# Kernel tuning notes

Hardware: AMD Instinct MI355X
Metric: run time of the kernel (lower is better)

The kernel has to match this reference:

```python
import jax, jax.numpy as jnp
import numpy as np

B, L, D, H = 2, 2048, 2048, 16
HD = D // H          # head_dim = 128
LD = HD // 4         # latent_dim = 32


def _linear_params(key, fan_in, fan_out):
    kw, kb = jax.random.split(key)
    bound = 1.0 / np.sqrt(fan_in)
    W = jax.random.uniform(kw, (fan_in, fan_out), jnp.float32, -bound, bound)
    b = jax.random.uniform(kb, (fan_out,), jnp.float32, -bound, bound)
    return W, b


def setup_inputs() -> dict:
    key = jax.random.key(0)
    ks = jax.random.split(key, 12)
    x = jax.random.normal(ks[0], (B, L, D), jnp.float32)
    cos = jax.random.uniform(ks[1], (L, HD // 2), jnp.float32)
    sin = jax.random.uniform(ks[2], (L, HD // 2), jnp.float32)
    Wq, bq = _linear_params(ks[3], D, D)
    Wk, bk = _linear_params(ks[4], D, D)
    Wv, bv = _linear_params(ks[5], D, D)
    Wqc, bqc = _linear_params(ks[6], HD, LD)
    Wkc, bkc = _linear_params(ks[7], HD, LD)
    Wvc, bvc = _linear_params(ks[8], HD, LD)
    Wd, bd = _linear_params(ks[9], LD, HD)
    Wo, bo = _linear_params(ks[10], D, D)
    return dict(x=x, cos=cos, sin=sin, Wq=Wq, bq=bq, Wk=Wk, bk=bk, Wv=Wv, bv=bv,
                Wqc=Wqc, bqc=bqc, Wkc=Wkc, bkc=bkc, Wvc=Wvc, bvc=bvc,
                Wd=Wd, bd=bd, Wo=Wo, bo=bo)


def _apply_rope(q, k, cos, sin):
    # q, k: (B, H, L, HD); cos, sin: (L, HD//2) -> broadcast over B, H
    c = cos[None, None, :, :]
    s = sin[None, None, :, :]
    qe, qo = q[..., ::2], q[..., 1::2]
    ke, ko = k[..., ::2], k[..., 1::2]
    q_rot = jnp.stack([qe * c - qo * s, qe * s + qo * c], axis=-1).reshape(q.shape)
    k_rot = jnp.stack([ke * c - ko * s, ke * s + ko * c], axis=-1).reshape(k.shape)
    return q_rot, k_rot


def reference(x, cos, sin, Wq, bq, Wk, bk, Wv, bv,
              Wqc, bqc, Wkc, bkc, Wvc, bvc, Wd, bd, Wo, bo):
    b, l, d = x.shape
    # projections -> (B, H, L, HD)
    q = (x @ Wq + bq).reshape(b, l, H, HD).transpose(0, 2, 1, 3)
    k = (x @ Wk + bk).reshape(b, l, H, HD).transpose(0, 2, 1, 3)
    v = (x @ Wv + bv).reshape(b, l, H, HD).transpose(0, 2, 1, 3)
    q, k = _apply_rope(q, k, cos, sin)
    # low-rank compression into latent_dim
    qc = jnp.einsum('bhld,de->bhle', q, Wqc) + bqc
    kc = jnp.einsum('bhld,de->bhle', k, Wkc) + bkc
    vc = jnp.einsum('bhld,de->bhle', v, Wvc) + bvc
    scores = jnp.einsum('bhqe,bhke->bhqk', qc, kc) / np.sqrt(LD).astype(np.float32)
    causal = jnp.tril(jnp.ones((l, l), dtype=bool))  # True = keep
    scores = jnp.where(causal[None, None], scores, -jnp.inf)
    probs = jax.nn.softmax(scores, axis=-1)
    attn = jnp.einsum('bhqk,bhke->bhqe', probs, vc)
    attn = jnp.einsum('bhle,ed->bhld', attn, Wd) + bd  # decompress to HD
    attn = attn.transpose(0, 2, 1, 3).reshape(b, l, d)
    return attn @ Wo + bo
```

## Files before the change

kernel.cpp:

```cpp
#include <hip/hip_runtime.h>
#include <hip/hip_bf16.h>


#define Bsz 2
#define Lseq 2048
#define Dmod 2048
#define Hn 16
#define HDim 128
#define LDim 32

typedef __bf16 bf16x8 __attribute__((ext_vector_type(8)));
typedef float f32x4 __attribute__((ext_vector_type(4)));
typedef __hip_bfloat16 bf16;

#define GLDS16(g, l)                                                    \
  __builtin_amdgcn_global_load_lds(                                     \
      (const __attribute__((address_space(1))) unsigned int*)(g),       \
      (__attribute__((address_space(3))) unsigned int*)(l), 16, 0, 0)

#define SM_COS 0
#define SM_SIN 131072
#define SM_WC 262144
#define SM_BC 274432
#define SM_WD 274528
#define SM_BD 278624
#define SM_BO 278752
#define SM_BQKV 280800
#define SM_TOT 286944

__global__ void detect_dtype(const ushort* __restrict__ x, int* __restrict__ flag) {
  int t = threadIdx.x;
  int bad = 0;
  for (int k = 0; k < 4; ++k) {
    ushort u = x[t * 4 + k];
    int ex = (u >> 7) & 0xFF;
    if (ex >= 0xC0) bad = 1;
  }
  unsigned long long b = __ballot(bad);
  if (t == 0) *flag = (b != 0ULL) ? 1 : 0;
}

__device__ inline void conv8(const void* src, size_t so, bf16* dst, size_t dof, int f32) {
  if (f32) {
    const float* s = (const float*)src + so;
    bf16 tmp[8] __attribute__((aligned(16)));
    for (int j = 0; j < 8; ++j) tmp[j] = __float2bfloat16(s[j]);
    *(uint4*)&dst[dof] = *(uint4*)tmp;
  } else {
    *(uint4*)&dst[dof] = *(const uint4*)((const ushort*)src + so);
  }
}

__device__ inline float cv1(const void* s, size_t i, int f32) {
  return f32 ? ((const float*)s)[i] : __bfloat162float(((const bf16*)s)[i]);
}

__global__ __launch_bounds__(256) void conv_x(const void* __restrict__ xs,
                                              bf16* __restrict__ xd,
                                              const int* __restrict__ flagp) {
  int f32 = *flagp;
  size_t e = ((size_t)blockIdx.x * 256 + threadIdx.x) * 8;
  conv8(xs, e, xd, e, f32);
}

__global__ __launch_bounds__(256) void prep(
    const void* cosS, const void* sinS, const void* WqcS, const void* WkcS,
    const void* WvcS, const void* bqcS, const void* bkcS, const void* bvcS,
    const void* WdS, const void* bdS, const void* boS, const void* bqS,
    const void* bkS, const void* bvS, bf16* __restrict__ dst,
    bf16* __restrict__ wctG, bf16* __restrict__ wdtG,
    const int* __restrict__ flagp) {
  int f32 = *flagp;
  int tid = blockIdx.x * 256 + threadIdx.x;
  if (tid < SM_TOT / 8) {
    size_t e = (size_t)tid * 8;
    const void* src;
    size_t so;
    if (e < SM_SIN) { src = cosS; so = e - SM_COS; }
    else if (e < SM_WC) { src = sinS; so = e - SM_SIN; }
    else if (e < SM_BC) { size_t r = e - SM_WC; src = (r < 4096) ? WqcS : (r < 8192) ? WkcS : WvcS; so = r & 4095; }
    else if (e < SM_WD) { size_t r = e - SM_BC; src = (r < 32) ? bqcS : (r < 64) ? bkcS : bvcS; so = r & 31; }
    else if (e < SM_BD) { src = WdS; so = e - SM_WD; }
    else if (e < SM_BO) { src = bdS; so = e - SM_BD; }
    else if (e < SM_BQKV) { src = boS; so = e - SM_BO; }
    else { size_t r = e - SM_BQKV; src = (r < 2048) ? bqS : (r < 4096) ? bkS : bvS; so = r & 2047; }
    conv8(src, so, dst, e, f32);
  } else {
    int idx = tid - SM_TOT / 8;
    for (int i = idx; i < 16384; i += 40960 - SM_TOT / 8) {
      if (i < 12288) {
        int reg = i >> 12, rem = i & 4095, n = rem >> 7, k = rem & 127;
        const void* src = (reg == 0) ? WqcS : (reg == 1) ? WkcS : WvcS;
        wctG[i] = __float2bfloat16(cv1(src, (size_t)k * 32 + n, f32));
      } else {
        int i2 = i - 12288, o = i2 >> 5, e = i2 & 31;
        wdtG[i2] = __float2bfloat16(cv1(WdS, (size_t)e * 128 + o, f32));
      }
    }
  }
}

__global__ __launch_bounds__(256) void transpose3(const void* __restrict__ WqS,
                                                  const void* __restrict__ WkS,
                                                  const void* __restrict__ WoS,
                                                  bf16* __restrict__ WtQK,
                                                  bf16* __restrict__ WtO,
                                                  const int* __restrict__ flagp) {
  __shared__ float tile[64][65];
  int f32 = *flagp;
  int z = blockIdx.z;
  const void* W = (z == 0) ? WqS : (z == 1) ? WkS : WoS;
  bf16* Wt = (z == 2) ? WtO : (WtQK + (size_t)z * 2048 * 2048);
  int n0 = blockIdx.x * 64, k0 = blockIdx.y * 64;
  int t = threadIdx.x;
  int x = (t & 7) * 8, y = t >> 3;
  for (int p = 0; p < 2; ++p) {
    int r = y + p * 32;
    if (f32) {
      const float* src = (const float*)W + (size_t)(k0 + r) * 2048 + n0 + x;
      float4 a = *(const float4*)src;
      float4 b2 = *(const float4*)(src + 4);
      tile[r][x + 0] = a.x; tile[r][x + 1] = a.y; tile[r][x + 2] = a.z; tile[r][x + 3] = a.w;
      tile[r][x + 4] = b2.x; tile[r][x + 5] = b2.y; tile[r][x + 6] = b2.z; tile[r][x + 7] = b2.w;
    } else {
      const ushort* src = (const ushort*)W + (size_t)(k0 + r) * 2048 + n0 + x;
      uint4 u = *(const uint4*)src;
      bf16* e = (bf16*)&u;
      for (int j = 0; j < 8; ++j) tile[r][x + j] = __bfloat162float(e[j]);
    }
  }
  __syncthreads();
  for (int p = 0; p < 2; ++p) {
    int n = y + p * 32;
    bf16 tmp[8] __attribute__((aligned(16)));
    for (int j = 0; j < 8; ++j) tmp[j] = __float2bfloat16(tile[x + j][n]);
    *(uint4*)&Wt[(size_t)(n0 + n) * 2048 + k0 + x] = *(uint4*)tmp;
  }
}

__global__ __launch_bounds__(256) void fold_vw(const bf16* __restrict__ WvB,
                                               const bf16* __restrict__ wctG,
                                               bf16* __restrict__ Wvt) {
  int nb = blockIdx.x, h = blockIdx.y;
  int t = threadIdx.x, lane = t & 63, w = t >> 6;
  int qd = lane >> 4, ln = lane & 15;
  f32x4 acc[2][2] = {};
  for (int kt = 0; kt < 4; ++kt) {
    bf16x8 af[2], bfr[2];
    for (int i = 0; i < 2; ++i)
      af[i] = *(const bf16x8*)&wctG[8192 + (i * 16 + ln) * 128 + kt * 32 + qd * 8];
    for (int j = 0; j < 2; ++j)
      bfr[j] = *(const bf16x8*)&WvB[(size_t)(nb * 128 + w * 32 + j * 16 + ln) * 2048 +
                                    h * 128 + kt * 32 + qd * 8];
    for (int i = 0; i < 2; ++i)
      for (int j = 0; j < 2; ++j)
        acc[i][j] = __builtin_amdgcn_mfma_f32_16x16x32_bf16(af[i], bfr[j], acc[i][j], 0, 0, 0);
  }
  for (int i = 0; i < 2; ++i)
    for (int j = 0; j < 2; ++j)
      for (int r = 0; r < 4; ++r) {
        int e = i * 16 + qd * 4 + r;
        int col = nb * 128 + w * 32 + j * 16 + ln;
        Wvt[(size_t)(h * 32 + e) * 2048 + col] = __float2bfloat16(acc[i][j][r]);
      }
}

__global__ __launch_bounds__(256) void fold_ow(const bf16* __restrict__ WtO,
                                               const bf16* __restrict__ small,
                                               bf16* __restrict__ Wot) {
  int mb = blockIdx.x, h = blockIdx.y;
  int t = threadIdx.x, lane = t & 63, w = t >> 6;
  int qd = lane >> 4, ln = lane & 15;
  f32x4 acc[2][2] = {};
  for (int kt = 0; kt < 4; ++kt) {
    bf16x8 af[2], bfr[2];
    for (int i = 0; i < 2; ++i)
      af[i] = *(const bf16x8*)&WtO[(size_t)(mb * 128 + w * 32 + i * 16 + ln) * 2048 +
                                   h * 128 + kt * 32 + qd * 8];
    for (int j = 0; j < 2; ++j)
      bfr[j] = *(const bf16x8*)&small[SM_WD + (j * 16 + ln) * 128 + kt * 32 + qd * 8];
    for (int i = 0; i < 2; ++i)
      for (int j = 0; j < 2; ++j)
        acc[i][j] = __builtin_amdgcn_mfma_f32_16x16x32_bf16(af[i], bfr[j], acc[i][j], 0, 0, 0);
  }
  for (int i = 0; i < 2; ++i)
    for (int j = 0; j < 2; ++j)
      for (int r = 0; r < 4; ++r) {
        int row = mb * 128 + w * 32 + i * 16 + qd * 4 + r;
        int col = h * 32 + j * 16 + ln;
        Wot[(size_t)row * 512 + col] = __float2bfloat16(acc[i][j][r]);
      }
}

__global__ __launch_bounds__(256) void fold_bias_partial(const void* WoS, const void* bdS,
                                                         float* __restrict__ bo_part,
                                                         const int* __restrict__ flagp) {
  __shared__ float red[256];
  int f32 = *flagp;
  int nb = blockIdx.x, kb = blockIdx.y;
  int t = threadIdx.x;
  int col = nb * 128 + (t & 127);
  int half = t >> 7;
  float s = 0.f;
  int kbase = kb * 128 + half * 64;
  for (int i = 0; i < 64; ++i) {
    int k = kbase + i;
    s += cv1(bdS, k & 127, f32) * cv1(WoS, (size_t)k * 2048 + col, f32);
  }
  red[t] = s;
  __syncthreads();
  if (half == 0) bo_part[kb * 2048 + col] = red[t] + red[t + 128];
}

__global__ __launch_bounds__(256) void fold_bias_final(const void* boS,
                                                       const float* __restrict__ bo_part,
                                                       const void* bvS, const void* bvcS,
                                                       const void* WvcS,
                                                       float* __restrict__ boF,
                                                       float* __restrict__ bvF,
                                                       const int* __restrict__ flagp) {
  int f32 = *flagp;
  int tid = blockIdx.x * 256 + threadIdx.x;
  if (tid < 2048) {
    float s = cv1(boS, tid, f32);
    for (int kb = 0; kb < 16; ++kb) s += bo_part[kb * 2048 + tid];
    boF[tid] = s;
  } else if (tid < 2560) {
    int j = tid - 2048, h = j >> 5, e = j & 31;
    float s = cv1(bvcS, e, f32);
    for (int hd = 0; hd < 128; ++hd)
      s += cv1(bvS, h * 128 + hd, f32) * cv1(WvcS, (size_t)hd * 32 + e, f32);
    bvF[j] = s;
  }
}

#define ESTR 136
__global__ __launch_bounds__(256) void gemm_qk_compress(
    const bf16* __restrict__ A, const bf16* __restrict__ Bt,
    const bf16* __restrict__ small, const bf16* __restrict__ wctG,
    bf16* __restrict__ qc, bf16* __restrict__ kc) {
  __shared__ bf16 sh[128 * ESTR];
  bf16* lA = sh;
  bf16* lB = sh + 4096;
  const int K = 2048;
  int bm = blockIdx.y, bn = blockIdx.x;
  int reg = bn >> 4, h = bn & 15;
  int t = threadIdx.x;
  int lane = t & 63, w = t >> 6;
  int wm = (w >> 1) * 64, wn = (w & 1) * 64;
  int qd = lane >> 4, ln = lane & 15;

  f32x4 acc[4][4] = {};
  const bf16* Ab = A + (size_t)(bm * 128) * K;
  const bf16* Bb = Bt + (size_t)(bn * 128) * K;

  for (int kt = 0; kt < K; kt += 32) {
    for (int p = 0; p < 2; ++p) {
      int slot = t + p * 256;
      int r = slot >> 2, c = (slot & 3) * 8;
      GLDS16(&Ab[(size_t)r * K + kt + c], &lA[slot * 8]);
      GLDS16(&Bb[(size_t)r * K + kt + c], &lB[slot * 8]);
    }
    __syncthreads();
    bf16x8 af[4], bfr[4];
    for (int i = 0; i < 4; ++i) af[i] = *(bf16x8*)&lA[(wm + i * 16 + ln) * 32 + qd * 8];
    for (int j = 0; j < 4; ++j) bfr[j] = *(bf16x8*)&lB[(wn + j * 16 + ln) * 32 + qd * 8];
    for (int i = 0; i < 4; ++i)
      for (int j = 0; j < 4; ++j)
        acc[i][j] = __builtin_amdgcn_mfma_f32_16x16x32_bf16(af[i], bfr[j], acc[i][j], 0, 0, 0);
    __syncthreads();
  }

  for (int j = 0; j < 4; ++j) {
    int col = wn + j * 16 + ln;
    float bv = __bfloat162float(small[SM_BQKV + bn * 128 + col]);
    for (int i = 0; i < 4; ++i)
      for (int r = 0; r < 4; ++r)
        sh[(wm + i * 16 + qd * 4 + r) * ESTR + col] = __float2bfloat16(acc[i][j][r] + bv);
  }
  __syncthreads();

  int r0 = w * 32;
  int b = bm >> 4;
  int bh = b * Hn + h;
  bf16x8 bfr2[2][4];
  for (int nt = 0; nt < 2; ++nt)
    for (int kt = 0; kt < 4; ++kt)
      bfr2[nt][kt] = *(const bf16x8*)&wctG[reg * 4096 + (nt * 16 + ln) * 128 + kt * 32 + qd * 8];
  float bc[2];
  bc[0] = __bfloat162float(small[SM_BC + reg * 32 + ln]);
  bc[1] = __bfloat162float(small[SM_BC + reg * 32 + 16 + ln]);

  for (int mt = 0; mt < 2; ++mt) {
    int lb = r0 + mt * 16 + ln;
    int lg = (bm & 15) * 128 + lb;
    f32x4 c2[2] = {};
    for (int kt = 0; kt < 4; ++kt) {
      uint4 u = *(uint4*)&sh[lb * ESTR + kt * 32 + qd * 8];
      bf16* e8 = (bf16*)&u;
      int pbase = kt * 16 + qd * 4;
      for (int j = 0; j < 4; ++j) {
        float cvv = __bfloat162float(small[SM_COS + (size_t)lg * 64 + pbase + j]);
        float svv = __bfloat162float(small[SM_SIN + (size_t)lg * 64 + pbase + j]);
        float ev = __bfloat162float(e8[2 * j]);
        float ov = __bfloat162float(e8[2 * j + 1]);
        e8[2 * j] = __float2bfloat16(ev * cvv - ov * svv);
        e8[2 * j + 1] = __float2bfloat16(ev * svv + ov * cvv);
      }
      bf16x8 a = *(bf16x8*)&u;
      c2[0] = __builtin_amdgcn_mfma_f32_16x16x32_bf16(a, bfr2[0][kt], c2[0], 0, 0, 0);
      c2[1] = __builtin_amdgcn_mfma_f32_16x16x32_bf16(a, bfr2[1][kt], c2[1], 0, 0, 0);
    }
    int lgbase = (bm & 15) * 128 + r0 + mt * 16 + qd * 4;
    bf16* dst = (reg == 0) ? qc : kc;
    for (int nt = 0; nt < 2; ++nt)
      for (int r = 0; r < 4; ++r)
        dst[((size_t)bh * Lseq + lgbase + r) * 32 + nt * 16 + ln] =
            __float2bfloat16(c2[nt][r] + bc[nt]);
  }
}

__global__ __launch_bounds__(256) void gemm_v_fold(const bf16* __restrict__ A,
                                                   const bf16* __restrict__ Wvt,
                                                   const float* __restrict__ bvF,
                                                   bf16* __restrict__ vcT) {
  __shared__ bf16 lA[64 * 32];
  __shared__ bf16 lB[64 * 32];
  const int K = 2048;
  int bm = blockIdx.y, nb = blockIdx.x;
  int t = threadIdx.x;
  int lane = t & 63, w = t >> 6;
  int wm = (w >> 1) * 32, wn = (w & 1) * 32;
  int qd = lane >> 4, ln = lane & 15;

  f32x4 acc[2][2] = {};
  const bf16* Ab = A + (size_t)(bm * 64) * K;
  const bf16* Bb = Wvt + (size_t)(nb * 64) * K;

  int r = t >> 2, c = (t & 3) * 8;
  for (int kt = 0; kt < K; kt += 32) {
    GLDS16(&Ab[(size_t)r * K + kt + c], &lA[t * 8]);
    GLDS16(&Bb[(size_t)r * K + kt + c], &lB[t * 8]);
    __syncthreads();
    bf16x8 af[2], bfr[2];
    for (int i = 0; i < 2; ++i) af[i] = *(bf16x8*)&lA[(wm + i * 16 + ln) * 32 + qd * 8];
    for (int j = 0; j < 2; ++j) bfr[j] = *(bf16x8*)&lB[(wn + j * 16 + ln) * 32 + qd * 8];
    for (int i = 0; i < 2; ++i)
      for (int j = 0; j < 2; ++j)
        acc[i][j] = __builtin_amdgcn_mfma_f32_16x16x32_bf16(af[i], bfr[j], acc[i][j], 0, 0, 0);
    __syncthreads();
  }

  int b = bm >> 5;
  for (int j = 0; j < 2; ++j) {
    int n = nb * 64 + wn + j * 16 + ln;
    float bb = bvF[n];
    for (int i = 0; i < 2; ++i) {
      int lloc = (bm & 31) * 64 + wm + i * 16 + qd * 4;
      bf16 p4[4] __attribute__((aligned(8)));
      for (int rr = 0; rr < 4; ++rr) p4[rr] = __float2bfloat16(acc[i][j][rr] + bb);
      *(uint2*)&vcT[((size_t)(b * 512 + n)) * 2048 + lloc] = *(uint2*)p4;
    }
  }
}

__global__ __launch_bounds__(256) void gemm_bias_out(const bf16* __restrict__ A,
                                                     const bf16* __restrict__ Bt,
                                                     const float* __restrict__ bias,
                                                     void* __restrict__ C,
                                                     int M, int N, int K,
                                                     const int* __restrict__ flagp) {
  __shared__ bf16 lA[128 * 32];
  __shared__ bf16 lB[128 * 32];
  int f32out = *flagp;
  int bm = blockIdx.y, bn = blockIdx.x;
  int t = threadIdx.x;
  int lane = t & 63, w = t >> 6;
  int wm = (w >> 1) * 64, wn = (w & 1) * 64;
  int qd = lane >> 4, ln = lane & 15;

  f32x4 acc[4][4] = {};
  const bf16* Ab = A + (size_t)(bm * 128) * K;
  const bf16* Bb = Bt + (size_t)(bn * 128) * K;

  for (int kt = 0; kt < K; kt += 32) {
    for (int p = 0; p < 2; ++p) {
      int slot = t + p * 256;
      int r = slot >> 2, c = (slot & 3) * 8;
      GLDS16(&Ab[(size_t)r * K + kt + c], &lA[slot * 8]);
      GLDS16(&Bb[(size_t)r * K + kt + c], &lB[slot * 8]);
    }
    __syncthreads();
    bf16x8 af[4], bfr[4];
    for (int i = 0; i < 4; ++i) af[i] = *(bf16x8*)&lA[(wm + i * 16 + ln) * 32 + qd * 8];
    for (int j = 0; j < 4; ++j) bfr[j] = *(bf16x8*)&lB[(wn + j * 16 + ln) * 32 + qd * 8];
    for (int i = 0; i < 4; ++i)
      for (int j = 0; j < 4; ++j)
        acc[i][j] = __builtin_amdgcn_mfma_f32_16x16x32_bf16(af[i], bfr[j], acc[i][j], 0, 0, 0);
    __syncthreads();
  }
  for (int i = 0; i < 4; ++i)
    for (int j = 0; j < 4; ++j) {
      int col = bn * 128 + wn + j * 16 + ln;
      float bv = bias[col];
      for (int r = 0; r < 4; ++r) {
        int row = bm * 128 + wm + i * 16 + qd * 4 + r;
        float v = acc[i][j][r] + bv;
        if (f32out) ((float*)C)[(size_t)row * N + col] = v;
        else ((bf16*)C)[(size_t)row * N + col] = __float2bfloat16(v);
      }
    }
}

__global__ __launch_bounds__(256) void flash32(const bf16* __restrict__ qc,
                                               const bf16* __restrict__ kc,
                                               const bf16* __restrict__ vcT,
                                               bf16* __restrict__ attn) {
  __shared__ bf16 pbuf[4][16 * 40];
  __shared__ float oL[4][16][33];
  __shared__ float mL[4][16];
  __shared__ float lsL[4][16];
  int t = threadIdx.x;
  int lane = t & 63, w = t >> 6;
  int qd = lane >> 4, ln = lane & 15;
  int blk = blockIdx.x;
  int j = blk & 127;
  int bh = blk >> 7, h = bh & 15, b = bh >> 4;
  int q0 = j * 16;

  bf16x8 qf = *(const bf16x8*)&qc[((size_t)bh * Lseq + q0 + ln) * 32 + qd * 8];

  f32x4 o0 = {}, o1 = {};
  float m[4], ls[4];
  for (int r = 0; r < 4; ++r) { m[r] = -1e30f; ls[r] = 0.f; }
  const float scale = 0.17677669529663687f;

  int nkt = (16 * j + 47) >> 5;
  int nw = (nkt + 3) >> 2;
  int kt0 = w * nw;
  int kt1 = min(kt0 + nw, nkt);

  bf16* pb = pbuf[w];
  for (int kt = kt0; kt < kt1; ++kt) {
    int k0 = kt * 32;
    bf16x8 kf0 = *(const bf16x8*)&kc[((size_t)bh * Lseq + k0 + ln) * 32 + qd * 8];
    bf16x8 kf1 = *(const bf16x8*)&kc[((size_t)bh * Lseq + k0 + 16 + ln) * 32 + qd * 8];
    f32x4 s0 = {}, s1 = {};
    s0 = __builtin_amdgcn_mfma_f32_16x16x32_bf16(qf, kf0, s0, 0, 0, 0);
    s1 = __builtin_amdgcn_mfma_f32_16x16x32_bf16(qf, kf1, s1, 0, 0, 0);
    float sv0[4], sv1[4], alpha[4];
    for (int r = 0; r < 4; ++r) {
      int qrow = q0 + qd * 4 + r;
      sv0[r] = (k0 + ln <= qrow) ? s0[r] * scale : -1e30f;
      sv1[r] = (k0 + 16 + ln <= qrow) ? s1[r] * scale : -1e30f;
    }
    for (int r = 0; r < 4; ++r) {
      float mx = fmaxf(sv0[r], sv1[r]);
      for (int off = 1; off < 16; off <<= 1) mx = fmaxf(mx, __shfl_xor(mx, off, 64));
      float mn = fmaxf(m[r], mx);
      alpha[r] = __expf(m[r] - mn);
      m[r] = mn;
      sv0[r] = __expf(sv0[r] - mn);
      sv1[r] = __expf(sv1[r] - mn);
      ls[r] = ls[r] * alpha[r] + sv0[r] + sv1[r];
      o0[r] *= alpha[r];
      o1[r] *= alpha[r];
    }
    for (int r = 0; r < 4; ++r) {
      pb[(qd * 4 + r) * 40 + ln] = __float2bfloat16(sv0[r]);
      pb[(qd * 4 + r) * 40 + 16 + ln] = __float2bfloat16(sv1[r]);
    }
    asm volatile("s_waitcnt lgkmcnt(0)" ::: "memory");
    bf16x8 pf = *(bf16x8*)&pb[ln * 40 + qd * 8];
    bf16x8 vf0 = *(const bf16x8*)&vcT[((size_t)bh * 32 + ln) * Lseq + k0 + qd * 8];
    bf16x8 vf1 = *(const bf16x8*)&vcT[((size_t)bh * 32 + 16 + ln) * Lseq + k0 + qd * 8];
    o0 = __builtin_amdgcn_mfma_f32_16x16x32_bf16(pf, vf0, o0, 0, 0, 0);
    o1 = __builtin_amdgcn_mfma_f32_16x16x32_bf16(pf, vf1, o1, 0, 0, 0);
  }

  for (int r = 0; r < 4; ++r)
    for (int off = 1; off < 16; off <<= 1) ls[r] += __shfl_xor(ls[r], off, 64);

  for (int r = 0; r < 4; ++r) {
    int row = qd * 4 + r;
    oL[w][row][ln] = o0[r];
    oL[w][row][16 + ln] = o1[r];
    if (ln == 0) { mL[w][row] = m[r]; lsL[w][row] = ls[r]; }
  }
  __syncthreads();

  for (int idx = t; idx < 512; idx += 256) {
    int row = idx >> 5, col = idx & 31;
    float m0 = mL[0][row], m1 = mL[1][row], m2 = mL[2][row], m3 = mL[3][row];
    float ms = fmaxf(fmaxf(m0, m1), fmaxf(m2, m3));
    float e0 = __expf(m0 - ms), e1 = __expf(m1 - ms);
    float e2 = __expf(m2 - ms), e3 = __expf(m3 - ms);
    float lsum = lsL[0][row] * e0 + lsL[1][row] * e1 + lsL[2][row] * e2 + lsL[3][row] * e3;
    float val = oL[0][row][col] * e0 + oL[1][row][col] * e1 +
                oL[2][row][col] * e2 + oL[3][row][col] * e3;
    int l = q0 + row;
    attn[((size_t)(b * Lseq + l)) * 512 + h * 32 + col] = __float2bfloat16(val / lsum);
  }
}

extern "C" void kernel_launch(void* const* d_in, const int* in_sizes, int n_in,
                              void* d_out, int out_size, void* d_ws, size_t ws_size,
                              hipStream_t stream) {
  const void* x = d_in[0];
  const void* cosS = d_in[1];
  const void* sinS = d_in[2];
  const void* Wq = d_in[3];
  const void* bq = d_in[4];
  const void* Wk = d_in[5];
  const void* bk = d_in[6];
  const void* Wv = d_in[7];
  const void* bv = d_in[8];
  const void* Wqc = d_in[9];
  const void* bqc = d_in[10];
  const void* Wkc = d_in[11];
  const void* bkc = d_in[12];
  const void* Wvc = d_in[13];
  const void* bvc = d_in[14];
  const void* Wd = d_in[15];
  const void* bd = d_in[16];
  const void* Wo = d_in[17];
  const void* bo = d_in[18];

  char* ws = (char*)d_ws;
  size_t off = 0;
  auto alloc = [&](size_t bytes) {
    char* p = ws + off;
    off += (bytes + 255) & ~(size_t)255;
    return p;
  };
  int* flag = (int*)alloc(256);
  bf16* small = (bf16*)alloc((size_t)SM_TOT * 2);
  bf16* wctG = (bf16*)alloc((size_t)12288 * 2);
  bf16* wdtG = (bf16*)alloc((size_t)4096 * 2);
  bf16* xb = (bf16*)alloc((size_t)4096 * 2048 * 2);
  bf16* WvB = (bf16*)alloc((size_t)2048 * 2048 * 2);
  bf16* WtQK = (bf16*)alloc((size_t)4096 * 2048 * 2);
  bf16* WtO = (bf16*)alloc((size_t)2048 * 2048 * 2);
  bf16* Wvt = (bf16*)alloc((size_t)512 * 2048 * 2);
  bf16* Wot = (bf16*)alloc((size_t)2048 * 512 * 2);
  float* bo_part = (float*)alloc((size_t)16 * 2048 * 4);
  float* boF = (float*)alloc((size_t)2048 * 4);
  float* bvF = (float*)alloc((size_t)512 * 4);
  bf16* qcW = (bf16*)alloc((size_t)65536 * 32 * 2);
  bf16* kcW = (bf16*)alloc((size_t)65536 * 32 * 2);
  bf16* vcTW = (bf16*)alloc((size_t)65536 * 32 * 2);
  bf16* attnW = (bf16*)alloc((size_t)4096 * 512 * 2);

  dim3 tb(256);
  detect_dtype<<<1, 64, 0, stream>>>((const ushort*)x, flag);
  prep<<<160, tb, 0, stream>>>(cosS, sinS, Wqc, Wkc, Wvc, bqc, bkc, bvc, Wd, bd, bo, bq,
                               bk, bv, small, wctG, wdtG, flag);
  transpose3<<<dim3(32, 32, 3), tb, 0, stream>>>(Wq, Wk, Wo, WtQK, WtO, flag);
  conv_x<<<4096, tb, 0, stream>>>(x, xb, flag);
  conv_x<<<2048, tb, 0, stream>>>(Wv, WvB, flag);
  fold_vw<<<dim3(16, 16), tb, 0, stream>>>(WvB, wctG, Wvt);
  fold_ow<<<dim3(16, 16), tb, 0, stream>>>(WtO, small, Wot);
  fold_bias_partial<<<dim3(16, 16), tb, 0, stream>>>(Wo, bd, bo_part, flag);
  fold_bias_final<<<10, tb, 0, stream>>>(bo, bo_part, bv, bvc, Wvc, boF, bvF, flag);
  gemm_v_fold<<<dim3(8, 64), tb, 0, stream>>>(xb, Wvt, bvF, vcTW);
  gemm_qk_compress<<<dim3(32, 32), tb, 0, stream>>>(xb, WtQK, small, wctG, qcW, kcW);
  flash32<<<4096, tb, 0, stream>>>(qcW, kcW, vcTW, attnW);
  gemm_bias_out<<<dim3(16, 32), tb, 0, stream>>>(attnW, Wot, boF, d_out, 4096, 2048,
                                                 512, flag);
}
```

Measured before the change: 429.7 us.

## Merge prep kernels, swizzle QK GEMM blocks, widen flash key tile to 64

Eight small preprocessing launches are merged into two kernels (prep_all and fold_all) that dispatch on block index, cutting launch overhead and serialization between them. The QK-compress GEMM now uses a 1D grid with a block-index swizzle so neighbouring blocks share A/B tiles for better cache reuse. The flash attention inner loop processes 64 keys per iteration instead of 32, halving the softmax reduction and LDS round-trips per key. The order of the V and QK GEMM launches is also swapped. Merging kernels raises per-kernel register and shared-memory usage to the largest branch, and the wider flash tile increases register pressure.

Result: faster. 409.1 us (-4.8%).

```diff
diff --git a/kernel.cpp b/kernel.cpp
--- a/kernel.cpp
+++ b/kernel.cpp
@@ -55,182 +55,176 @@
   return f32 ? ((const float*)s)[i] : __bfloat162float(((const bf16*)s)[i]);
 }
 
-__global__ __launch_bounds__(256) void conv_x(const void* __restrict__ xs,
-                                              bf16* __restrict__ xd,
-                                              const int* __restrict__ flagp) {
+#define NB_T3 3072
+#define NB_WV 2048
+#define NB_CX 4096
+#define NB_PREP 160
+#define NB_FBP 256
+#define NB_PREP_ALL (NB_T3 + NB_WV + NB_CX + NB_PREP + NB_FBP)
+
+__global__ __launch_bounds__(256) void prep_all(
+    const void* xS, const void* cosS, const void* sinS, const void* WqS,
+    const void* WkS, const void* WvS, const void* WoS, const void* WqcS,
+    const void* WkcS, const void* WvcS, const void* bqcS, const void* bkcS,
+    const void* bvcS, const void* WdS, const void* bdS, const void* boS,
+    const void* bqS, const void* bkS, const void* bvS,
+    bf16* __restrict__ xb, bf16* __restrict__ WvB, bf16* __restrict__ WtQK,
+    bf16* __restrict__ WtO, bf16* __restrict__ small, bf16* __restrict__ wctG,
+    bf16* __restrict__ wdtG, float* __restrict__ bo_part,
+    const int* __restrict__ flagp) {
+  __shared__ __align__(16) char shm[16640];
   int f32 = *flagp;
-  size_t e = ((size_t)blockIdx.x * 256 + threadIdx.x) * 8;
-  conv8(xs, e, xd, e, f32);
-}
-
-__global__ __launch_bounds__(256) void prep(
-    const void* cosS, const void* sinS, const void* WqcS, const void* WkcS,
-    const void* WvcS, const void* bqcS, const void* bkcS, const void* bvcS,
-    const void* WdS, const void* bdS, const void* boS, const void* bqS,
-    const void* bkS, const void* bvS, bf16* __restrict__ dst,
-    bf16* __restrict__ wctG, bf16* __restrict__ wdtG,
+  int blk = blockIdx.x;
+  int t = threadIdx.x;
+
+  if (blk < NB_T3) {
+    float (*tile)[65] = (float(*)[65])shm;
+    int z = blk >> 10, rem = blk & 1023;
+    const void* W = (z == 0) ? WqS : (z == 1) ? WkS : WoS;
+    bf16* Wt = (z == 2) ? WtO : (WtQK + (size_t)z * 2048 * 2048);
+    int n0 = (rem & 31) * 64, k0 = (rem >> 5) * 64;
+    int x = (t & 7) * 8, y = t >> 3;
+    for (int p = 0; p < 2; ++p) {
+      int r = y + p * 32;
+      if (f32) {
+        const float* src = (const float*)W + (size_t)(k0 + r) * 2048 + n0 + x;
+        float4 a = *(const float4*)src;
+        float4 b2 = *(const float4*)(src + 4);
+        tile[r][x + 0] = a.x; tile[r][x + 1] = a.y; tile[r][x + 2] = a.z; tile[r][x + 3] = a.w;
+        tile[r][x + 4] = b2.x; tile[r][x + 5] = b2.y; tile[r][x + 6] = b2.z; tile[r][x + 7] = b2.w;
+      } else {
+        const ushort* src = (const ushort*)W + (size_t)(k0 + r) * 2048 + n0 + x;
+        uint4 u = *(const uint4*)src;
+        bf16* e = (bf16*)&u;
+        for (int jj = 0; jj < 8; ++jj) tile[r][x + jj] = __bfloat162float(e[jj]);
+      }
+    }
+    __syncthreads();
+    for (int p = 0; p < 2; ++p) {
+      int n = y + p * 32;
+      bf16 tmp[8] __attribute__((aligned(16)));
+      for (int jj = 0; jj < 8; ++jj) tmp[jj] = __float2bfloat16(tile[x + jj][n]);
+      *(uint4*)&Wt[(size_t)(n0 + n) * 2048 + k0 + x] = *(uint4*)tmp;
+    }
+  } else if (blk < NB_T3 + NB_WV) {
+    size_t e = ((size_t)(blk - NB_T3) * 256 + t) * 8;
+    conv8(WvS, e, WvB, e, f32);
+  } else if (blk < NB_T3 + NB_WV + NB_CX) {
+    size_t e = ((size_t)(blk - NB_T3 - NB_WV) * 256 + t) * 8;
+    conv8(xS, e, xb, e, f32);
+  } else if (blk < NB_T3 + NB_WV + NB_CX + NB_PREP) {
+    int tid = (blk - NB_T3 - NB_WV - NB_CX) * 256 + t;
+    if (tid < SM_TOT / 8) {
+      size_t e = (size_t)tid * 8;
+      const void* src;
+      size_t so;
+      if (e < SM_SIN) { src = cosS; so = e - SM_COS; }
+      else if (e < SM_WC) { src = sinS; so = e - SM_SIN; }
+      else if (e < SM_BC) { size_t r = e - SM_WC; src = (r < 4096) ? WqcS : (r < 8192) ? WkcS : WvcS; so = r & 4095; }
+      else if (e < SM_WD) { size_t r = e - SM_BC; src = (r < 32) ? bqcS : (r < 64) ? bkcS : bvcS; so = r & 31; }
+      else if (e < SM_BD) { src = WdS; so = e - SM_WD; }
+      else if (e < SM_BO) { src = bdS; so = e - SM_BD; }
+      else if (e < SM_BQKV) { src = boS; so = e - SM_BO; }
+      else { size_t r = e - SM_BQKV; src = (r < 2048) ? bqS : (r < 4096) ? bkS : bvS; so = r & 2047; }
+      conv8(src, so, small, e, f32);
+    } else {
+      int idx = tid - SM_TOT / 8;
+      for (int i = idx; i < 16384; i += 40960 - SM_TOT / 8) {
+        if (i < 12288) {
+          int reg = i >> 12, rem2 = i & 4095, n = rem2 >> 7, k = rem2 & 127;
+          const void* src = (reg == 0) ? WqcS : (reg == 1) ? WkcS : WvcS;
+          wctG[i] = __float2bfloat16(cv1(src, (size_t)k * 32 + n, f32));
+        } else {
+          int i2 = i - 12288, o = i2 >> 5, e = i2 & 31;
+          wdtG[i2] = __float2bfloat16(cv1(WdS, (size_t)e * 128 + o, f32));
+        }
+      }
+    }
+  } else {
+    float* red = (float*)shm;
+    int rem = blk - (NB_T3 + NB_WV + NB_CX + NB_PREP);
+    int nb = rem & 15, kb = rem >> 4;
+    int col = nb * 128 + (t & 127);
+    int half = t >> 7;
+    float s = 0.f;
+    int kbase = kb * 128 + half * 64;
+    for (int i = 0; i < 64; ++i) {
+      int k = kbase + i;
+      s += cv1(bdS, k & 127, f32) * cv1(WoS, (size_t)k * 2048 + col, f32);
+    }
+    red[t] = s;
+    __syncthreads();
+    if (half == 0) bo_part[kb * 2048 + col] = red[t] + red[t + 128];
+  }
+}
+
+__global__ __launch_bounds__(256) void fold_all(
+    const bf16* __restrict__ WvB, const bf16* __restrict__ wctG,
+    const bf16* __restrict__ WtO, const bf16* __restrict__ small,
+    const void* boS, const float* __restrict__ bo_part, const void* bvS,
+    const void* bvcS, const void* WvcS, bf16* __restrict__ Wvt,
+    bf16* __restrict__ Wot, float* __restrict__ boF, float* __restrict__ bvF,
     const int* __restrict__ flagp) {
-  int f32 = *flagp;
-  int tid = blockIdx.x * 256 + threadIdx.x;
-  if (tid < SM_TOT / 8) {
-    size_t e = (size_t)tid * 8;
-    const void* src;
-    size_t so;
-    if (e < SM_SIN) { src = cosS; so = e - SM_COS; }
-    else if (e < SM_WC) { src = sinS; so = e - SM_SIN; }
-    else if (e < SM_BC) { size_t r = e - SM_WC; src = (r < 4096) ? WqcS : (r < 8192) ? WkcS : WvcS; so = r & 4095; }
-    else if (e < SM_WD) { size_t r = e - SM_BC; src = (r < 32) ? bqcS : (r < 64) ? bkcS : bvcS; so = r & 31; }
-    else if (e < SM_BD) { src = WdS; so = e - SM_WD; }
-    else if (e < SM_BO) { src = bdS; so = e - SM_BD; }
-    else if (e < SM_BQKV) { src = boS; so = e - SM_BO; }
-    else { size_t r = e - SM_BQKV; src = (r < 2048) ? bqS : (r < 4096) ? bkS : bvS; so = r & 2047; }
-    conv8(src, so, dst, e, f32);
-  } else {
-    int idx = tid - SM_TOT / 8;
-    for (int i = idx; i < 16384; i += 40960 - SM_TOT / 8) {
-      if (i < 12288) {
-        int reg = i >> 12, rem = i & 4095, n = rem >> 7, k = rem & 127;
-        const void* src = (reg == 0) ? WqcS : (reg == 1) ? WkcS : WvcS;
-        wctG[i] = __float2bfloat16(cv1(src, (size_t)k * 32 + n, f32));
-      } else {
-        int i2 = i - 12288, o = i2 >> 5, e = i2 & 31;
-        wdtG[i2] = __float2bfloat16(cv1(WdS, (size_t)e * 128 + o, f32));
-      }
-    }
-  }
-}
-
-__global__ __launch_bounds__(256) void transpose3(const void* __restrict__ WqS,
-                                                  const void* __restrict__ WkS,
-                                                  const void* __restrict__ WoS,
-                                                  bf16* __restrict__ WtQK,
-                                                  bf16* __restrict__ WtO,
-                                                  const int* __restrict__ flagp) {
-  __shared__ float tile[64][65];
-  int f32 = *flagp;
-  int z = blockIdx.z;
-  const void* W = (z == 0) ? WqS : (z == 1) ? WkS : WoS;
-  bf16* Wt = (z == 2) ? WtO : (WtQK + (size_t)z * 2048 * 2048);
-  int n0 = blockIdx.x * 64, k0 = blockIdx.y * 64;
-  int t = threadIdx.x;
-  int x = (t & 7) * 8, y = t >> 3;
-  for (int p = 0; p < 2; ++p) {
-    int r = y + p * 32;
-    if (f32) {
-      const float* src = (const float*)W + (size_t)(k0 + r) * 2048 + n0 + x;
-      float4 a = *(const float4*)src;
-      float4 b2 = *(const float4*)(src + 4);
-      tile[r][x + 0] = a.x; tile[r][x + 1] = a.y; tile[r][x + 2] = a.z; tile[r][x + 3] = a.w;
-      tile[r][x + 4] = b2.x; tile[r][x + 5] = b2.y; tile[r][x + 6] = b2.z; tile[r][x + 7] = b2.w;
-    } else {
-      const ushort* src = (const ushort*)W + (size_t)(k0 + r) * 2048 + n0 + x;
-      uint4 u = *(const uint4*)src;
-      bf16* e = (bf16*)&u;
-      for (int j = 0; j < 8; ++j) tile[r][x + j] = __bfloat162float(e[j]);
-    }
-  }
-  __syncthreads();
-  for (int p = 0; p < 2; ++p) {
-    int n = y + p * 32;
-    bf16 tmp[8] __attribute__((aligned(16)));
-    for (int j = 0; j < 8; ++j) tmp[j] = __float2bfloat16(tile[x + j][n]);
-    *(uint4*)&Wt[(size_t)(n0 + n) * 2048 + k0 + x] = *(uint4*)tmp;
-  }
-}
-
-__global__ __launch_bounds__(256) void fold_vw(const bf16* __restrict__ WvB,
-                                               const bf16* __restrict__ wctG,
-                                               bf16* __restrict__ Wvt) {
-  int nb = blockIdx.x, h = blockIdx.y;
+  int blk = blockIdx.x;
   int t = threadIdx.x, lane = t & 63, w = t >> 6;
   int qd = lane >> 4, ln = lane & 15;
-  f32x4 acc[2][2] = {};
-  for (int kt = 0; kt < 4; ++kt) {
-    bf16x8 af[2], bfr[2];
-    for (int i = 0; i < 2; ++i)
-      af[i] = *(const bf16x8*)&wctG[8192 + (i * 16 + ln) * 128 + kt * 32 + qd * 8];
-    for (int j = 0; j < 2; ++j)
-      bfr[j] = *(const bf16x8*)&WvB[(size_t)(nb * 128 + w * 32 + j * 16 + ln) * 2048 +
-                                    h * 128 + kt * 32 + qd * 8];
+  if (blk < 256) {
+    int nb = blk & 15, h = blk >> 4;
+    f32x4 acc[2][2] = {};
+    for (int kt = 0; kt < 4; ++kt) {
+      bf16x8 af[2], bfr[2];
+      for (int i = 0; i < 2; ++i)
+        af[i] = *(const bf16x8*)&wctG[8192 + (i * 16 + ln) * 128 + kt * 32 + qd * 8];
+      for (int j = 0; j < 2; ++j)
+        bfr[j] = *(const bf16x8*)&WvB[(size_t)(nb * 128 + w * 32 + j * 16 + ln) * 2048 +
+                                      h * 128 + kt * 32 + qd * 8];
+      for (int i = 0; i < 2; ++i)
+        for (int j = 0; j < 2; ++j)
+          acc[i][j] = __builtin_amdgcn_mfma_f32_16x16x32_bf16(af[i], bfr[j], acc[i][j], 0, 0, 0);
+    }
     for (int i = 0; i < 2; ++i)
       for (int j = 0; j < 2; ++j)
-        acc[i][j] = __builtin_amdgcn_mfma_f32_16x16x32_bf16(af[i], bfr[j], acc[i][j], 0, 0, 0);
-  }
-  for (int i = 0; i < 2; ++i)
-    for (int j = 0; j < 2; ++j)
-      for (int r = 0; r < 4; ++r) {
-        int e = i * 16 + qd * 4 + r;
-        int col = nb * 128 + w * 32 + j * 16 + ln;
-        Wvt[(size_t)(h * 32 + e) * 2048 + col] = __float2bfloat16(acc[i][j][r]);
-      }
-}
-
-__global__ __launch_bounds__(256) void fold_ow(const bf16* __restrict__ WtO,
-                                               const bf16* __restrict__ small,
-                                               bf16* __restrict__ Wot) {
-  int mb = blockIdx.x, h = blockIdx.y;
-  int t = threadIdx.x, lane = t & 63, w = t >> 6;
-  int qd = lane >> 4, ln = lane & 15;
-  f32x4 acc[2][2] = {};
-  for (int kt = 0; kt < 4; ++kt) {
-    bf16x8 af[2], bfr[2];
-    for (int i = 0; i < 2; ++i)
-      af[i] = *(const bf16x8*)&WtO[(size_t)(mb * 128 + w * 32 + i * 16 + ln) * 2048 +
-                                   h * 128 + kt * 32 + qd * 8];
-    for (int j = 0; j < 2; ++j)
-      bfr[j] = *(const bf16x8*)&small[SM_WD + (j * 16 + ln) * 128 + kt * 32 + qd * 8];
+        for (int r = 0; r < 4; ++r) {
+          int e = i * 16 + qd * 4 + r;
+          int col = nb * 128 + w * 32 + j * 16 + ln;
+          Wvt[(size_t)(h * 32 + e) * 2048 + col] = __float2bfloat16(acc[i][j][r]);
+        }
+  } else if (blk < 512) {
+    int rem = blk - 256;
+    int mb = rem & 15, h = rem >> 4;
+    f32x4 acc[2][2] = {};
+    for (int kt = 0; kt < 4; ++kt) {
+      bf16x8 af[2], bfr[2];
+      for (int i = 0; i < 2; ++i)
+        af[i] = *(const bf16x8*)&WtO[(size_t)(mb * 128 + w * 32 + i * 16 + ln) * 2048 +
+                                     h * 128 + kt * 32 + qd * 8];
+      for (int j = 0; j < 2; ++j)
+        bfr[j] = *(const bf16x8*)&small[SM_WD + (j * 16 + ln) * 128 + kt * 32 + qd * 8];
+      for (int i = 0; i < 2; ++i)
+        for (int j = 0; j < 2; ++j)
+          acc[i][j] = __builtin_amdgcn_mfma_f32_16x16x32_bf16(af[i], bfr[j], acc[i][j], 0, 0, 0);
+    }
     for (int i = 0; i < 2; ++i)
       for (int j = 0; j < 2; ++j)
-        acc[i][j] = __builtin_amdgcn_mfma_f32_16x16x32_bf16(af[i], bfr[j], acc[i][j], 0, 0, 0);
-  }
-  for (int i = 0; i < 2; ++i)
-    for (int j = 0; j < 2; ++j)
-      for (int r = 0; r < 4; ++r) {
-        int row = mb * 128 + w * 32 + i * 16 + qd * 4 + r;
-        int col = h * 32 + j * 16 + ln;
-        Wot[(size_t)row * 512 + col] = __float2bfloat16(acc[i][j][r]);
-      }
-}
-
-__global__ __launch_bounds__(256) void fold_bias_partial(const void* WoS, const void* bdS,
-                                                         float* __restrict__ bo_part,
-                                                         const int* __restrict__ flagp) {
-  __shared__ float red[256];
-  int f32 = *flagp;
-  int nb = blockIdx.x, kb = blockIdx.y;
-  int t = threadIdx.x;
-  int col = nb * 128 + (t & 127);
-  int half = t >> 7;
-  float s = 0.f;
-  int kbase = kb * 128 + half * 64;
-  for (int i = 0; i < 64; ++i) {
-    int k = kbase + i;
-    s += cv1(bdS, k & 127, f32) * cv1(WoS, (size_t)k * 2048 + col, f32);
-  }
-  red[t] = s;
-  __syncthreads();
-  if (half == 0) bo_part[kb * 2048 + col] = red[t] + red[t + 128];
-}
-
-__global__ __launch_bounds__(256) void fold_bias_final(const void* boS,
-                                                       const float* __restrict__ bo_part,
-                                                       const void* bvS, const void* bvcS,
-                                                       const void* WvcS,
-                                                       float* __restrict__ boF,
-                                                       float* __restrict__ bvF,
-                                                       const int* __restrict__ flagp) {
-  int f32 = *flagp;
-  int tid = blockIdx.x * 256 + threadIdx.x;
-  if (tid < 2048) {
-    float s = cv1(boS, tid, f32);
-    for (int kb = 0; kb < 16; ++kb) s += bo_part[kb * 2048 + tid];
-    boF[tid] = s;
-  } else if (tid < 2560) {
-    int j = tid - 2048, h = j >> 5, e = j & 31;
-    float s = cv1(bvcS, e, f32);
-    for (int hd = 0; hd < 128; ++hd)
-      s += cv1(bvS, h * 128 + hd, f32) * cv1(WvcS, (size_t)hd * 32 + e, f32);
-    bvF[j] = s;
+        for (int r = 0; r < 4; ++r) {
+          int row = mb * 128 + w * 32 + i * 16 + qd * 4 + r;
+          int col = h * 32 + j * 16 + ln;
+          Wot[(size_t)row * 512 + col] = __float2bfloat16(acc[i][j][r]);
+        }
+  } else {
+    int f32 = *flagp;
+    int tid = (blk - 512) * 256 + t;
+    if (tid < 2048) {
+      float s = cv1(boS, tid, f32);
+      for (int kb = 0; kb < 16; ++kb) s += bo_part[kb * 2048 + tid];
+      boF[tid] = s;
+    } else if (tid < 2560) {
+      int j = tid - 2048, h = j >> 5, e = j & 31;
+      float s = cv1(bvcS, e, f32);
+      for (int hd = 0; hd < 128; ++hd)
+        s += cv1(bvS, h * 128 + hd, f32) * cv1(WvcS, (size_t)hd * 32 + e, f32);
+      bvF[j] = s;
+    }
   }
 }
 
@@ -243,7 +237,9 @@
   bf16* lA = sh;
   bf16* lB = sh + 4096;
   const int K = 2048;
-  int bm = blockIdx.y, bn = blockIdx.x;
+  int id = blockIdx.x;
+  int lg = (id & 7) * 128 + (id >> 3);
+  int bm = lg >> 5, bn = lg & 31;
   int reg = bn >> 4, h = bn & 15;
   int t = threadIdx.x;
   int lane = t & 63, w = t >> 6;
@@ -293,15 +289,15 @@
 
   for (int mt = 0; mt < 2; ++mt) {
     int lb = r0 + mt * 16 + ln;
-    int lg = (bm & 15) * 128 + lb;
+    int lg2 = (bm & 15) * 128 + lb;
     f32x4 c2[2] = {};
     for (int kt = 0; kt < 4; ++kt) {
       uint4 u = *(uint4*)&sh[lb * ESTR + kt * 32 + qd * 8];
       bf16* e8 = (bf16*)&u;
       int pbase = kt * 16 + qd * 4;
       for (int j = 0; j < 4; ++j) {
-        float cvv = __bfloat162float(small[SM_COS + (size_t)lg * 64 + pbase + j]);
-        float svv = __bfloat162float(small[SM_SIN + (size_t)lg * 64 + pbase + j]);
+        float cvv = __bfloat162float(small[SM_COS + (size_t)lg2 * 64 + pbase + j]);
+        float svv = __bfloat162float(small[SM_SIN + (size_t)lg2 * 64 + pbase + j]);
         float ev = __bfloat162float(e8[2 * j]);
         float ov = __bfloat162float(e8[2 * j + 1]);
         e8[2 * j] = __float2bfloat16(ev * cvv - ov * svv);
@@ -416,7 +412,7 @@
                                                const bf16* __restrict__ kc,
                                                const bf16* __restrict__ vcT,
                                                bf16* __restrict__ attn) {
-  __shared__ bf16 pbuf[4][16 * 40];
+  __shared__ bf16 pbuf[4][16 * 72];
   __shared__ float oL[4][16][33];
   __shared__ float mL[4][16];
   __shared__ float lsL[4][16];
@@ -435,47 +431,52 @@
   for (int r = 0; r < 4; ++r) { m[r] = -1e30f; ls[r] = 0.f; }
   const float scale = 0.17677669529663687f;
 
-  int nkt = (16 * j + 47) >> 5;
-  int nw = (nkt + 3) >> 2;
-  int kt0 = w * nw;
-  int kt1 = min(kt0 + nw, nkt);
+  int n64 = (q0 + 16 + 63) >> 6;
+  int nw = (n64 + 3) >> 2;
+  int c0 = w * nw;
+  int c1 = min(c0 + nw, n64);
 
   bf16* pb = pbuf[w];
-  for (int kt = kt0; kt < kt1; ++kt) {
-    int k0 = kt * 32;
-    bf16x8 kf0 = *(const bf16x8*)&kc[((size_t)bh * Lseq + k0 + ln) * 32 + qd * 8];
-    bf16x8 kf1 = *(const bf16x8*)&kc[((size_t)bh * Lseq + k0 + 16 + ln) * 32 + qd * 8];
-    f32x4 s0 = {}, s1 = {};
-    s0 = __builtin_amdgcn_mfma_f32_16x16x32_bf16(qf, kf0, s0, 0, 0, 0);
-    s1 = __builtin_amdgcn_mfma_f32_16x16x32_bf16(qf, kf1, s1, 0, 0, 0);
-    float sv0[4], sv1[4], alpha[4];
+  for (int ci = c0; ci < c1; ++ci) {
+    int k0 = ci * 64;
+    f32x4 s[4];
+    for (int c = 0; c < 4; ++c) {
+      bf16x8 kf = *(const bf16x8*)&kc[((size_t)bh * Lseq + k0 + c * 16 + ln) * 32 + qd * 8];
+      f32x4 z = {};
+      s[c] = __builtin_amdgcn_mfma_f32_16x16x32_bf16(qf, kf, z, 0, 0, 0);
+    }
+    float sv[4][4], alpha[4];
     for (int r = 0; r < 4; ++r) {
       int qrow = q0 + qd * 4 + r;
-      sv0[r] = (k0 + ln <= qrow) ? s0[r] * scale : -1e30f;
-      sv1[r] = (k0 + 16 + ln <= qrow) ? s1[r] * scale : -1e30f;
+      for (int c = 0; c < 4; ++c)
+        sv[c][r] = (k0 + c * 16 + ln <= qrow) ? s[c][r] * scale : -1e30f;
     }
     for (int r = 0; r < 4; ++r) {
-      float mx = fmaxf(sv0[r], sv1[r]);
+      float mx = fmaxf(fmaxf(sv[0][r], sv[1][r]), fmaxf(sv[2][r], sv[3][r]));
       for (int off = 1; off < 16; off <<= 1) mx = fmaxf(mx, __shfl_xor(mx, off, 64));
       float mn = fmaxf(m[r], mx);
       alpha[r] = __expf(m[r] - mn);
       m[r] = mn;
-      sv0[r] = __expf(sv0[r] - mn);
-      sv1[r] = __expf(sv1[r] - mn);
-      ls[r] = ls[r] * alpha[r] + sv0[r] + sv1[r];
+      float rs = 0.f;
+      for (int c = 0; c < 4; ++c) { sv[c][r] = __expf(sv[c][r] - mn); rs += sv[c][r]; }
+      ls[r] = ls[r] * alpha[r] + rs;
       o0[r] *= alpha[r];
       o1[r] *= alpha[r];
     }
-    for (int r = 0; r < 4; ++r) {
-      pb[(qd * 4 + r) * 40 + ln] = __float2bfloat16(sv0[r]);
-      pb[(qd * 4 + r) * 40 + 16 + ln] = __float2bfloat16(sv1[r]);
-    }
+    for (int r = 0; r < 4; ++r)
+      for (int c = 0; c < 4; ++c)
+        pb[(qd * 4 + r) * 72 + c * 16 + ln] = __float2bfloat16(sv[c][r]);
     asm volatile("s_waitcnt lgkmcnt(0)" ::: "memory");
-    bf16x8 pf = *(bf16x8*)&pb[ln * 40 + qd * 8];
-    bf16x8 vf0 = *(const bf16x8*)&vcT[((size_t)bh * 32 + ln) * Lseq + k0 + qd * 8];
-    bf16x8 vf1 = *(const bf16x8*)&vcT[((size_t)bh * 32 + 16 + ln) * Lseq + k0 + qd * 8];
-    o0 = __builtin_amdgcn_mfma_f32_16x16x32_bf16(pf, vf0, o0, 0, 0, 0);
-    o1 = __builtin_amdgcn_mfma_f32_16x16x32_bf16(pf, vf1, o1, 0, 0, 0);
+    bf16x8 pf0 = *(bf16x8*)&pb[ln * 72 + qd * 8];
+    bf16x8 pf1 = *(bf16x8*)&pb[ln * 72 + 32 + qd * 8];
+    bf16x8 vf00 = *(const bf16x8*)&vcT[((size_t)bh * 32 + ln) * Lseq + k0 + qd * 8];
+    bf16x8 vf01 = *(const bf16x8*)&vcT[((size_t)bh * 32 + ln) * Lseq + k0 + 32 + qd * 8];
+    bf16x8 vf10 = *(const bf16x8*)&vcT[((size_t)bh * 32 + 16 + ln) * Lseq + k0 + qd * 8];
+    bf16x8 vf11 = *(const bf16x8*)&vcT[((size_t)bh * 32 + 16 + ln) * Lseq + k0 + 32 + qd * 8];
+    o0 = __builtin_amdgcn_mfma_f32_16x16x32_bf16(pf0, vf00, o0, 0, 0, 0);
+    o0 = __builtin_amdgcn_mfma_f32_16x16x32_bf16(pf1, vf01, o0, 0, 0, 0);
+    o1 = __builtin_amdgcn_mfma_f32_16x16x32_bf16(pf0, vf10, o1, 0, 0, 0);
+    o1 = __builtin_amdgcn_mfma_f32_16x16x32_bf16(pf1, vf11, o1, 0, 0, 0);
   }
 
   for (int r = 0; r < 4; ++r)
@@ -553,17 +554,13 @@
 
   dim3 tb(256);
   detect_dtype<<<1, 64, 0, stream>>>((const ushort*)x, flag);
-  prep<<<160, tb, 0, stream>>>(cosS, sinS, Wqc, Wkc, Wvc, bqc, bkc, bvc, Wd, bd, bo, bq,
-                               bk, bv, small, wctG, wdtG, flag);
-  transpose3<<<dim3(32, 32, 3), tb, 0, stream>>>(Wq, Wk, Wo, WtQK, WtO, flag);
-  conv_x<<<4096, tb, 0, stream>>>(x, xb, flag);
-  conv_x<<<2048, tb, 0, stream>>>(Wv, WvB, flag);
-  fold_vw<<<dim3(16, 16), tb, 0, stream>>>(WvB, wctG, Wvt);
-  fold_ow<<<dim3(16, 16), tb, 0, stream>>>(WtO, small, Wot);
-  fold_bias_partial<<<dim3(16, 16), tb, 0, stream>>>(Wo, bd, bo_part, flag);
-  fold_bias_final<<<10, tb, 0, stream>>>(bo, bo_part, bv, bvc, Wvc, boF, bvF, flag);
+  prep_all<<<NB_PREP_ALL, tb, 0, stream>>>(
+      x, cosS, sinS, Wq, Wk, Wv, Wo, Wqc, Wkc, Wvc, bqc, bkc, bvc, Wd, bd, bo,
+      bq, bk, bv, xb, WvB, WtQK, WtO, small, wctG, wdtG, bo_part, flag);
+  fold_all<<<522, tb, 0, stream>>>(WvB, wctG, WtO, small, bo, bo_part, bv, bvc,
+                                   Wvc, Wvt, Wot, boF, bvF, flag);
+  gemm_qk_compress<<<1024, tb, 0, stream>>>(xb, WtQK, small, wctG, qcW, kcW);
   gemm_v_fold<<<dim3(8, 64), tb, 0, stream>>>(xb, Wvt, bvF, vcTW);
-  gemm_qk_compress<<<dim3(32, 32), tb, 0, stream>>>(xb, WtQK, small, wctG, qcW, kcW);
   flash32<<<4096, tb, 0, stream>>>(qcW, kcW, vcTW, attnW);
   gemm_bias_out<<<dim3(16, 32), tb, 0, stream>>>(attnW, Wot, boF, d_out, 4096, 2048,
                                                  512, flag);
```
